# Kernel optimization log

Hardware: AMD Instinct MI355X
Metric: run time of the kernel (lower is better)

Reference implementation:

```python
import jax, jax.numpy as jnp
import numpy as np
import math

N_HEAD = 16
N_HEAD_KV = 4
HEAD_DIM = 128
N_EMBD = 2048

def alibi_slopes(n_heads):
    def pow2_slopes(n):
        start = 2 ** (-2 ** (-(math.log2(n) - 3)))
        return [start * start ** i for i in range(n)]
    if math.log2(n_heads).is_integer():
        return jnp.array(pow2_slopes(n_heads), dtype=jnp.float32)
    closest = 2 ** math.floor(math.log2(n_heads))
    base = pow2_slopes(closest)
    if n_heads <= 2 * closest:
        s = base + base[0::2]
    else:
        s = base + base[0::2] + base[1::2]
    return jnp.array(s[:n_heads], dtype=jnp.float32)

def setup_inputs() -> dict:
    key = jax.random.key(0)
    ks = jax.random.split(key, 5)
    B, T, C = 2, 2048, N_EMBD
    kvdim = N_HEAD_KV * HEAD_DIM
    sc = 0.02
    return {
        "x": jax.random.normal(ks[0], (B, T, C), dtype=jnp.float32),
        "q_w": jax.random.normal(ks[1], (C, C), dtype=jnp.float32) * sc,
        "k_w": jax.random.normal(ks[2], (kvdim, C), dtype=jnp.float32) * sc,
        "v_w": jax.random.normal(ks[3], (kvdim, C), dtype=jnp.float32) * sc,
        "o_w": jax.random.normal(ks[4], (C, C), dtype=jnp.float32) * sc,
    }

def reference(x, q_w, k_w, v_w, o_w):
    B, T, C = x.shape
    H, Hkv, D = N_HEAD, N_HEAD_KV, HEAD_DIM
    # nan/inf sanitize (no-op for random inputs, kept for fidelity)
    x = jnp.nan_to_num(x, nan=0.0, posinf=10000.0, neginf=-10000.0)
    q = (x @ q_w.T).reshape(B, T, H, D).transpose(0, 2, 1, 3)      # [B,H,T,D]
    k = (x @ k_w.T).reshape(B, T, Hkv, D).transpose(0, 2, 1, 3)    # [B,Hkv,T,D]
    v = (x @ v_w.T).reshape(B, T, Hkv, D).transpose(0, 2, 1, 3)
    # repeat_interleave KV heads to H heads
    rep = H // Hkv
    k = jnp.repeat(k, rep, axis=1)
    v = jnp.repeat(v, rep, axis=1)
    scale = 1.0 / math.sqrt(D)
    att = jnp.einsum('bhqd,bhkd->bhqk', q, k) * scale
    att = jnp.clip(att, -10000.0, 10000.0)
    pos = jnp.arange(T)
    causal = jnp.where(pos[None, :] > pos[:, None], -jnp.inf, 0.0)  # [T,T]
    slopes = alibi_slopes(H)  # [H]
    rel = (pos[None, :] - pos[:, None]).astype(jnp.float32)         # [T,T]
    alibi = slopes[:, None, None] * rel[None]                        # [H,T,T]
    att = att + causal[None, None] + alibi[None]
    att = jax.nn.softmax(att.astype(jnp.float32), axis=-1).astype(q.dtype)
    y = jnp.einsum('bhqk,bhkd->bhqd', att, v)
    y = jnp.nan_to_num(y, nan=0.0, posinf=10000.0, neginf=-10000.0)
    y = y.transpose(0, 2, 1, 3).reshape(B, T, C)
    return y @ o_w.T
```

## Files before the change

kernel.cpp:

```cpp
#include <hip/hip_runtime.h>
#include <hip/hip_bf16.h>
#include <math.h>

#define SEQ   2048
#define EMBD  2048
#define NH    16
#define NKV   4
#define HD    128
#define NQKV  3072
#define NUNITS 608
#define NSPLIT 96

typedef __attribute__((ext_vector_type(8))) short short8;
typedef __attribute__((ext_vector_type(4))) short short4v;
typedef __attribute__((ext_vector_type(4))) float floatx4;

static __device__ __forceinline__ short f2bf(float f) {
    union { float f; unsigned u; } cv; cv.f = f;
    unsigned u = cv.u;
    u += 0x7FFF + ((u >> 16) & 1);
    return (short)(u >> 16);
}

#define GL16(gsrc, ldst)                                                        \
    __builtin_amdgcn_global_load_lds(                                           \
        (const __attribute__((address_space(1))) void*)(gsrc),                  \
        (__attribute__((address_space(3))) void*)(ldst), 16, 0, 0)

static __device__ __forceinline__ int alibi_window(float slope2) {
    return (int)ceilf((32.0f / slope2 + 63.0f) * (1.0f / 64.0f));
}

__global__ void cvt_all(const float* __restrict__ x,  const float* __restrict__ qw,
                        const float* __restrict__ kw, const float* __restrict__ vw,
                        const float* __restrict__ ow,
                        short* __restrict__ xb, short* __restrict__ wall,
                        short* __restrict__ owb) {
    int i = blockIdx.x * blockDim.x + threadIdx.x;
    const float* src; short* dst; int off;
    if (i < 2097152)      { src = x;  dst = xb;             off = i; }
    else if (i < 3145728) { src = qw; dst = wall;           off = i - 2097152; }
    else if (i < 3407872) { src = kw; dst = wall + 4194304; off = i - 3145728; }
    else if (i < 3670016) { src = vw; dst = wall + 5242880; off = i - 3407872; }
    else                  { src = ow; dst = owb;            off = i - 3670016; }
    float4 v = ((const float4*)src)[off];
    float a[4] = {v.x, v.y, v.z, v.w};
    short4v o;
#pragma unroll
    for (int j = 0; j < 4; ++j) {
        float f = a[j];
        f = isnan(f) ? 0.0f : fminf(fmaxf(f, -10000.0f), 10000.0f);
        o[j] = f2bf(f);
    }
    ((short4v*)dst)[off] = o;
}

__global__ void attn_setup(int* __restrict__ qtab) {
    __shared__ int keys[NUNITS];
    const int i = threadIdx.x;
    int key = 0, enc = 0;
    if (i < NUNITS) {
        int b, h, p, c;
        if (i < 512) { b = i >> 8; h = (i >> 4) & 15; p = i & 15; c = 0; }
        else { int j = i - 512; b = j / 48; int r2 = j % 48; h = 10 + r2 / 8; p = 8 + r2 % 8; c = 1; }
        float slope2 = exp2f(-0.5f * (float)(h + 1)) * 1.44269504f;
        int W = alibi_window(slope2);
        int L = min(W + 1, 2 * p + 2);
        bool split = (h >= 10) && (p >= 8);
        int n0 = (L + 1) >> 1;
        int cost = split ? (c == 0 ? n0 : L - n0) : L;
        enc = (c << 9) | (b << 8) | (h << 4) | p;
        key = cost * 1024 + i;
        keys[i] = key;
    }
    __syncthreads();
    if (i < NUNITS) {
        int rank = 0;
        for (int j = 0; j < NUNITS; ++j) rank += (keys[j] > key);
        qtab[rank] = enc;
    }
    if (i == 0) qtab[NUNITS] = 0;
}

template<int MODE>
__global__ __launch_bounds__(256) void gemm_bt(
    const short* __restrict__ A, const short* __restrict__ W,
    float* __restrict__ Cout, int M, int N, int K,
    short* __restrict__ qb, short* __restrict__ kb, short* __restrict__ vb)
{
    __shared__ __align__(16) short sA[128 * 64];
    __shared__ __align__(16) short sB[128 * 64];

    const int tid  = threadIdx.x;
    const int lane = tid & 63;
    const int wv   = tid >> 6;
    const int wr   = wv >> 1, wc = wv & 1;
    const int lr   = lane & 15, lg = lane >> 4;
    const int bn   = blockIdx.x, bm = blockIdx.y;

    const short* gA[4]; const short* gB[4];
    short* lA[4]; short* lB[4];
#pragma unroll
    for (int s = 0; s < 4; ++s) {
        int ck  = wv * 256 + s * 64 + lane;
        int row = ck >> 3, seg = ck & 7;
        int segSw = seg ^ (row & 7);
        gA[s] = A + (size_t)(bm * 128 + row) * K + segSw * 8;
        gB[s] = W + (size_t)(bn * 128 + row) * K + segSw * 8;
        lA[s] = &sA[(wv * 256 + s * 64) * 8];
        lB[s] = &sB[(wv * 256 + s * 64) * 8];
    }

    floatx4 acc[4][4] = {};
    const int nkt = K / 64;
    for (int kt = 0; kt < nkt; ++kt) {
#pragma unroll
        for (int s = 0; s < 4; ++s) {
            GL16(gA[s] + kt * 64, lA[s]);
            GL16(gB[s] + kt * 64, lB[s]);
        }
        __syncthreads();

#pragma unroll
        for (int ks = 0; ks < 2; ++ks) {
            short8 af[4], bfr[4];
#pragma unroll
            for (int i = 0; i < 4; ++i) {
                int ra = wr * 64 + i * 16 + lr;
                int rb = wc * 64 + i * 16 + lr;
                af[i]  = *(const short8*)&sA[ra * 64 + (((ks * 4 + lg) ^ (ra & 7)) * 8)];
                bfr[i] = *(const short8*)&sB[rb * 64 + (((ks * 4 + lg) ^ (rb & 7)) * 8)];
            }
#pragma unroll
            for (int i = 0; i < 4; ++i)
#pragma unroll
                for (int j = 0; j < 4; ++j)
                    acc[i][j] = __builtin_amdgcn_mfma_f32_16x16x32_bf16(af[i], bfr[j], acc[i][j], 0, 0, 0);
        }
        __syncthreads();
    }

    const float QSCALE = 0.08838834764831845f * 1.44269504f;
#pragma unroll
    for (int i = 0; i < 4; ++i)
#pragma unroll
        for (int j = 0; j < 4; ++j)
#pragma unroll
            for (int r = 0; r < 4; ++r) {
                int gm = bm * 128 + wr * 64 + i * 16 + lg * 4 + r;
                int gn = bn * 128 + wc * 64 + j * 16 + lr;
                float v = acc[i][j][r];
                if (MODE == 0) {
                    int b = gm >> 11, t = gm & (SEQ - 1);
                    if (gn < 2048) {
                        int h = gn >> 7, d = gn & 127;
                        qb[(((size_t)(b * NH + h)) * SEQ + t) * HD + d] = f2bf(v * QSCALE);
                    } else if (gn < 2560) {
                        int hk = (gn - 2048) >> 7, d = gn & 127;
                        kb[(((size_t)(b * NKV + hk)) * SEQ + t) * HD + d] = f2bf(v);
                    } else {
                        int hv = (gn - 2560) >> 7, d = gn & 127;
                        vb[(((size_t)(b * NKV + hv)) * HD + d) * SEQ + t] = f2bf(v);
                    }
                } else {
                    Cout[(size_t)gm * N + gn] = v;
                }
            }
}

__global__ __launch_bounds__(512, 4) void attn_fwd(
    const short* __restrict__ Q, const short* __restrict__ Kg,
    const short* __restrict__ VT, short* __restrict__ Y,
    float* __restrict__ part, int* __restrict__ qtab)
{
    __shared__ __align__(16) short sK[2][64 * 128];
    __shared__ __align__(16) short sV[128 * 64];
    __shared__ short Plds[8][16][72];
    __shared__ int s_unit;

    const int tid  = threadIdx.x;
    const int wave = tid >> 6, lane = tid & 63;
    const int lr = lane & 15, lg = lane >> 4;
    int* qcnt = qtab + NUNITS;

    int lOff[2];
#pragma unroll
    for (int j = 0; j < 2; ++j)
        lOff[j] = (wave * 128 + j * 64 + lane) * 8;

    for (;;) {
        if (tid == 0) {
            int r = atomicAdd(qcnt, 1);
            s_unit = (r < NUNITS) ? qtab[r] : -1;
        }
        __syncthreads();
        const int enc = s_unit;
        __syncthreads();
        if (enc < 0) break;

        const int c = (enc >> 9) & 1, b = (enc >> 8) & 1;
        const int h = (enc >> 4) & 15, p = enc & 15;
        const int hkv = h >> 2;
        const int qgw = 2 * p + (wave < 4 ? 1 : 0);

        const short* Qb = Q  +  ((size_t)(b * NH  + h  )) * SEQ * HD;
        const short* Kp = Kg +  ((size_t)(b * NKV + hkv)) * SEQ * HD;
        const short* Vp = VT +  ((size_t)(b * NKV + hkv)) * HD * SEQ;

        const float slope2 = exp2f(-0.5f * (float)(h + 1)) * 1.44269504f;
        const int W = alibi_window(slope2);
        const int thi = 2 * p + 1;
        const int L = min(W + 1, 2 * p + 2);
        const bool split = (h >= 10) && (p >= 8);
        const int n0 = (L + 1) >> 1;
        int t1, t0;
        if (!split)      { t1 = thi;      t0 = thi - L + 1; }
        else if (c == 0) { t1 = thi;      t0 = thi - n0 + 1; }
        else             { t1 = thi - n0; t0 = thi - L + 1; }

        const short* gK[2]; const short* gV[2];
#pragma unroll
        for (int j = 0; j < 2; ++j) {
            int ck = wave * 128 + j * 64 + lane;
            int krow = ck >> 4, kseg = ck & 15;
            gK[j] = Kp + (size_t)krow * HD + (kseg ^ (krow & 7)) * 8;
            int vrow = ck >> 3, vseg = ck & 7;
            gV[j] = Vp + (size_t)vrow * SEQ + (vseg ^ (vrow & 7)) * 8;
        }

        float c_nt[4];
#pragma unroll
        for (int nt = 0; nt < 4; ++nt) c_nt[nt] = slope2 * (float)(nt * 16 + lr);

        const int q0 = qgw * 64 + (wave & 3) * 16;
        short8 qf[4];
#pragma unroll
        for (int cc = 0; cc < 4; ++cc)
            qf[cc] = *(const short8*)&Qb[(size_t)(q0 + lr) * HD + cc * 32 + lg * 8];

        floatx4 po[8] = {};
        float m[4], lsum[4];
#pragma unroll
        for (int r = 0; r < 4; ++r) { m[r] = -3.0e38f; lsum[r] = 0.0f; }

        int cur = 0;
#pragma unroll
        for (int j = 0; j < 2; ++j)
            GL16(gK[j] + (size_t)(t1 << 6) * HD, &sK[0][0] + lOff[j]);
        __syncthreads();

#pragma unroll 1
        for (int t = t1; t >= t0; --t) {
#pragma unroll
            for (int j = 0; j < 2; ++j)
                GL16(gV[j] + (t << 6), &sV[0] + lOff[j]);
            if (t > t0) {
#pragma unroll
                for (int j = 0; j < 2; ++j)
                    GL16(gK[j] + (size_t)((t - 1) << 6) * HD, &sK[cur ^ 1][0] + lOff[j]);
            }

            const bool active = (t <= qgw) && (t > qgw - W);
            const int kv0 = t << 6;

            if (active) {
                const short* kr = &sK[cur][0];
                floatx4 sf[4];
                __builtin_amdgcn_s_setprio(1);
#pragma unroll
                for (int nt = 0; nt < 4; ++nt) {
                    floatx4 sacc = {0.f, 0.f, 0.f, 0.f};
#pragma unroll
                    for (int cc = 0; cc < 4; ++cc) {
                        int krow = nt * 16 + lr;
                        short8 kf = *(const short8*)&kr[krow * 128 + (((cc * 4 + lg) ^ (krow & 7)) * 8)];
                        sacc = __builtin_amdgcn_mfma_f32_16x16x32_bf16(qf[cc], kf, sacc, 0, 0, 0);
                    }
                    sf[nt] = sacc;
                }
                __builtin_amdgcn_s_setprio(0);

                const float a2t = slope2 * (float)kv0;
                const bool masked = (t == qgw);
#pragma unroll
                for (int r = 0; r < 4; ++r) {
                    const int qpos = q0 + lg * 4 + r;
                    float sv[4];
#pragma unroll
                    for (int nt = 0; nt < 4; ++nt)
                        sv[nt] = sf[nt][r] + a2t + c_nt[nt];
                    if (masked) {
#pragma unroll
                        for (int nt = 0; nt < 4; ++nt) {
                            int kpos = kv0 + nt * 16 + lr;
                            if (kpos > qpos) sv[nt] = -3.0e38f;
                        }
                    }
                    bool over = (sv[0] > m[r]) | (sv[1] > m[r]) | (sv[2] > m[r]) | (sv[3] > m[r]);
                    if (__any(over)) {
                        float mx = fmaxf(fmaxf(sv[0], sv[1]), fmaxf(sv[2], sv[3]));
#pragma unroll
                        for (int off = 1; off < 16; off <<= 1) mx = fmaxf(mx, __shfl_xor(mx, off));
                        float mn = fmaxf(m[r], mx);
                        float rs = exp2f(m[r] - mn);
                        lsum[r] *= rs;
#pragma unroll
                        for (int dt = 0; dt < 8; ++dt) po[dt][r] *= rs;
                        m[r] = mn;
                    }
#pragma unroll
                    for (int nt = 0; nt < 4; ++nt) {
                        float pp = exp2f(sv[nt] - m[r]);
                        lsum[r] += pp;
                        Plds[wave][lg * 4 + r][nt * 16 + lr] = f2bf(pp);
                    }
                }
            }

            __syncthreads();

            if (active) {
                short8 pf0 = *(const short8*)&Plds[wave][lr][lg * 8];
                short8 pf1 = *(const short8*)&Plds[wave][lr][32 + lg * 8];
                __builtin_amdgcn_s_setprio(1);
#pragma unroll
                for (int dt = 0; dt < 8; ++dt) {
                    int vrow = dt * 16 + lr;
                    short8 vf0 = *(const short8*)&sV[vrow * 64 + (((lg    ) ^ (vrow & 7)) * 8)];
                    short8 vf1 = *(const short8*)&sV[vrow * 64 + (((lg + 4) ^ (vrow & 7)) * 8)];
                    po[dt] = __builtin_amdgcn_mfma_f32_16x16x32_bf16(pf0, vf0, po[dt], 0, 0, 0);
                    po[dt] = __builtin_amdgcn_mfma_f32_16x16x32_bf16(pf1, vf1, po[dt], 0, 0, 0);
                }
                __builtin_amdgcn_s_setprio(0);
            }

            __syncthreads();
            cur ^= 1;
        }

        if (!split) {
#pragma unroll
            for (int r = 0; r < 4; ++r) {
                float sum = lsum[r];
#pragma unroll
                for (int off = 1; off < 16; off <<= 1) sum += __shfl_xor(sum, off);
                float inv = 1.0f / sum;
                int row = q0 + lg * 4 + r;
#pragma unroll
                for (int dt = 0; dt < 8; ++dt)
                    Y[((size_t)(b * SEQ + row)) * EMBD + h * HD + dt * 16 + lr] = f2bf(po[dt][r] * inv);
            }
        } else {
            int jslot = b * 48 + (h - 10) * 8 + (p - 8);
            float* pw = part + (size_t)(jslot * 2 + c) * (128 * 130);
#pragma unroll
            for (int r = 0; r < 4; ++r) {
                float sum = lsum[r];
#pragma unroll
                for (int off = 1; off < 16; off <<= 1) sum += __shfl_xor(sum, off);
                int rr = wave * 16 + lg * 4 + r;
#pragma unroll
                for (int dt = 0; dt < 8; ++dt)
                    pw[rr * 130 + dt * 16 + lr] = po[dt][r];
                if (lr == 0) { pw[rr * 130 + 128] = m[r]; pw[rr * 130 + 129] = sum; }
            }
        }
    }
}

__global__ void attn_combine(const float* __restrict__ part, short* __restrict__ Y) {
    const int tid = threadIdx.x;
    const int rg  = blockIdx.x * 2 + (tid >> 7);
    const int col = tid & 127;
    const int j = rg >> 7, rr = rg & 127;
    const int b = j / 48; const int r2 = j % 48;
    const int h = 10 + r2 / 8, p = 8 + r2 % 8;

    const float* p0 = part + ((size_t)(j * 2) * 128 + rr) * 130;
    const float* p1 = p0 + 128 * 130;
    float m0 = p0[128], l0 = p0[129];
    float m1 = p1[128], l1 = p1[129];
    float M = fmaxf(m0, m1);
    float s0 = exp2f(m0 - M), s1 = exp2f(m1 - M);
    float v = (p0[col] * s0 + p1[col] * s1) / (l0 * s0 + l1 * s1);

    const int w = rr >> 4, i2 = rr & 15;
    const int grow = (w < 4 ? (2 * p + 1) : (2 * p)) * 64 + (w & 3) * 16 + i2;
    Y[((size_t)(b * SEQ + grow)) * EMBD + h * HD + col] = f2bf(v);
}

extern "C" void kernel_launch(void* const* d_in, const int* in_sizes, int n_in,
                              void* d_out, int out_size, void* d_ws, size_t ws_size,
                              hipStream_t stream) {
    const float* x   = (const float*)d_in[0];
    const float* q_w = (const float*)d_in[1];
    const float* k_w = (const float*)d_in[2];
    const float* v_w = (const float*)d_in[3];
    const float* o_w = (const float*)d_in[4];
    float* out = (float*)d_out;

    char* ws = (char*)d_ws;
    short* x_bf  = (short*)(ws);
    short* w_all = (short*)(ws + 16777216);
    short* o_wb  = (short*)(ws + 29360128);
    short* q_b   = (short*)(ws + 37748736);
    short* k_b   = (short*)(ws + 54525952);
    short* vT_b  = (short*)(ws + 58720256);
    short* y_b   = (short*)(ws + 62914560);
    int*   qtab  = (int*)(ws);
    float* part  = (float*)(ws + 65536);

    cvt_all<<<18432, 256, 0, stream>>>(x, q_w, k_w, v_w, o_w, x_bf, w_all, o_wb);

    gemm_bt<0><<<dim3(NQKV / 128, 4096 / 128), 256, 0, stream>>>(
        x_bf, w_all, nullptr, 4096, NQKV, EMBD, q_b, k_b, vT_b);

    attn_setup<<<1, 640, 0, stream>>>(qtab);
    attn_fwd<<<512, 512, 0, stream>>>(q_b, k_b, vT_b, y_b, part, qtab);
    attn_combine<<<6144, 256, 0, stream>>>(part, y_b);

    gemm_bt<1><<<dim3(EMBD / 128, 4096 / 128), 256, 0, stream>>>(
        y_b, o_wb, out, 4096, EMBD, EMBD, nullptr, nullptr, nullptr);
}
```

Before: 201.8 us.

## Double-buffer GEMM LDS tiles with 256x128 blocks and interleaved prefetch

The bf16 GEMM kernel now runs 512 threads on a 256x128 output tile, with the A and B tiles double-buffered in LDS. Global-to-LDS loads for the next k-step are split into chunks and issued between MFMA phases, with s_barrier and setprio around each MFMA burst. This is meant to hide global load latency behind compute and to cut the per-iteration syncthreads stall. In exchange it uses more LDS per block (96KB) and launches fewer blocks for the QKV and output projections, which could lower occupancy and wave count on the CUs.

```diff
diff --git a/kernel.cpp b/kernel.cpp
--- a/kernel.cpp
+++ b/kernel.cpp
@@ -26,6 +26,8 @@
     __builtin_amdgcn_global_load_lds(                                           \
         (const __attribute__((address_space(1))) void*)(gsrc),                  \
         (__attribute__((address_space(3))) void*)(ldst), 16, 0, 0)
+
+#define MFMA16(a, b, c) __builtin_amdgcn_mfma_f32_16x16x32_bf16(a, b, c, 0, 0, 0)
 
 static __device__ __forceinline__ int alibi_window(float slope2) {
     return (int)ceilf((32.0f / slope2 + 63.0f) * (1.0f / 64.0f));
@@ -83,13 +85,13 @@
 }
 
 template<int MODE>
-__global__ __launch_bounds__(256) void gemm_bt(
+__global__ __launch_bounds__(512) void gemm_bt(
     const short* __restrict__ A, const short* __restrict__ W,
     float* __restrict__ Cout, int M, int N, int K,
     short* __restrict__ qb, short* __restrict__ kb, short* __restrict__ vb)
 {
-    __shared__ __align__(16) short sA[128 * 64];
-    __shared__ __align__(16) short sB[128 * 64];
+    __shared__ __align__(16) short sA[2][256 * 64];
+    __shared__ __align__(16) short sB[2][128 * 64];
 
     const int tid  = threadIdx.x;
     const int lane = tid & 63;
@@ -98,46 +100,113 @@
     const int lr   = lane & 15, lg = lane >> 4;
     const int bn   = blockIdx.x, bm = blockIdx.y;
 
-    const short* gA[4]; const short* gB[4];
-    short* lA[4]; short* lB[4];
+    const short* gA[4]; const short* gB[2];
+    int aOff[4], bOff[2];
 #pragma unroll
     for (int s = 0; s < 4; ++s) {
-        int ck  = wv * 256 + s * 64 + lane;
+        int ck = s * 512 + tid;
         int row = ck >> 3, seg = ck & 7;
-        int segSw = seg ^ (row & 7);
-        gA[s] = A + (size_t)(bm * 128 + row) * K + segSw * 8;
-        gB[s] = W + (size_t)(bn * 128 + row) * K + segSw * 8;
-        lA[s] = &sA[(wv * 256 + s * 64) * 8];
-        lB[s] = &sB[(wv * 256 + s * 64) * 8];
+        gA[s] = A + (size_t)(bm * 256 + row) * K + (seg ^ (row & 7)) * 8;
+        aOff[s] = ck * 8;
+    }
+#pragma unroll
+    for (int s = 0; s < 2; ++s) {
+        int ck = s * 512 + tid;
+        int row = ck >> 3, seg = ck & 7;
+        gB[s] = W + (size_t)(bn * 128 + row) * K + (seg ^ (row & 7)) * 8;
+        bOff[s] = ck * 8;
     }
 
     floatx4 acc[4][4] = {};
     const int nkt = K / 64;
+
+#pragma unroll
+    for (int s = 0; s < 4; ++s) GL16(gA[s], &sA[0][0] + aOff[s]);
+#pragma unroll
+    for (int s = 0; s < 2; ++s) GL16(gB[s], &sB[0][0] + bOff[s]);
+    __syncthreads();
+
+#pragma unroll 1
     for (int kt = 0; kt < nkt; ++kt) {
-#pragma unroll
-        for (int s = 0; s < 4; ++s) {
-            GL16(gA[s] + kt * 64, lA[s]);
-            GL16(gB[s] + kt * 64, lB[s]);
+        const int cur = kt & 1;
+        const short* a_ = &sA[cur][0];
+        const short* b_ = &sB[cur][0];
+        short* an = &sA[cur ^ 1][0];
+        short* bnx = &sB[cur ^ 1][0];
+        const bool pf = (kt + 1 < nkt);
+        const int ko = (kt + 1) * 64;
+
+        short8 afA, afB, bfr[4];
+
+        {
+            int ra0 = wr * 64 + lr, ra1 = wr * 64 + 16 + lr;
+            afA = *(const short8*)&a_[ra0 * 64 + ((lg ^ (ra0 & 7)) * 8)];
+            afB = *(const short8*)&a_[ra1 * 64 + ((lg ^ (ra1 & 7)) * 8)];
+#pragma unroll
+            for (int j = 0; j < 4; ++j) {
+                int rb = wc * 64 + j * 16 + lr;
+                bfr[j] = *(const short8*)&b_[rb * 64 + ((lg ^ (rb & 7)) * 8)];
+            }
+            if (pf) { GL16(gA[0] + ko, an + aOff[0]); GL16(gA[1] + ko, an + aOff[1]); }
+            __builtin_amdgcn_s_barrier();
+            __builtin_amdgcn_s_setprio(1);
+#pragma unroll
+            for (int j = 0; j < 4; ++j) {
+                acc[0][j] = MFMA16(afA, bfr[j], acc[0][j]);
+                acc[1][j] = MFMA16(afB, bfr[j], acc[1][j]);
+            }
+            __builtin_amdgcn_s_setprio(0);
+            __builtin_amdgcn_s_barrier();
+        }
+        {
+            int ra2 = wr * 64 + 32 + lr, ra3 = wr * 64 + 48 + lr;
+            afA = *(const short8*)&a_[ra2 * 64 + ((lg ^ (ra2 & 7)) * 8)];
+            afB = *(const short8*)&a_[ra3 * 64 + ((lg ^ (ra3 & 7)) * 8)];
+            if (pf) { GL16(gA[2] + ko, an + aOff[2]); GL16(gA[3] + ko, an + aOff[3]); }
+            __builtin_amdgcn_s_barrier();
+            __builtin_amdgcn_s_setprio(1);
+#pragma unroll
+            for (int j = 0; j < 4; ++j) {
+                acc[2][j] = MFMA16(afA, bfr[j], acc[2][j]);
+                acc[3][j] = MFMA16(afB, bfr[j], acc[3][j]);
+            }
+            __builtin_amdgcn_s_setprio(0);
+            __builtin_amdgcn_s_barrier();
+        }
+        {
+            int ra0 = wr * 64 + lr, ra1 = wr * 64 + 16 + lr;
+            afA = *(const short8*)&a_[ra0 * 64 + (((4 + lg) ^ (ra0 & 7)) * 8)];
+            afB = *(const short8*)&a_[ra1 * 64 + (((4 + lg) ^ (ra1 & 7)) * 8)];
+#pragma unroll
+            for (int j = 0; j < 4; ++j) {
+                int rb = wc * 64 + j * 16 + lr;
+                bfr[j] = *(const short8*)&b_[rb * 64 + (((4 + lg) ^ (rb & 7)) * 8)];
+            }
+            if (pf) { GL16(gB[0] + ko, bnx + bOff[0]); GL16(gB[1] + ko, bnx + bOff[1]); }
+            __builtin_amdgcn_s_barrier();
+            __builtin_amdgcn_s_setprio(1);
+#pragma unroll
+            for (int j = 0; j < 4; ++j) {
+                acc[0][j] = MFMA16(afA, bfr[j], acc[0][j]);
+                acc[1][j] = MFMA16(afB, bfr[j], acc[1][j]);
+            }
+            __builtin_amdgcn_s_setprio(0);
+            __builtin_amdgcn_s_barrier();
+        }
+        {
+            int ra2 = wr * 64 + 32 + lr, ra3 = wr * 64 + 48 + lr;
+            afA = *(const short8*)&a_[ra2 * 64 + (((4 + lg) ^ (ra2 & 7)) * 8)];
+            afB = *(const short8*)&a_[ra3 * 64 + (((4 + lg) ^ (ra3 & 7)) * 8)];
+            __builtin_amdgcn_s_barrier();
+            __builtin_amdgcn_s_setprio(1);
+#pragma unroll
+            for (int j = 0; j < 4; ++j) {
+                acc[2][j] = MFMA16(afA, bfr[j], acc[2][j]);
+                acc[3][j] = MFMA16(afB, bfr[j], acc[3][j]);
+            }
+            __builtin_amdgcn_s_setprio(0);
         }
         __syncthreads();
-
-#pragma unroll
-        for (int ks = 0; ks < 2; ++ks) {
-            short8 af[4], bfr[4];
-#pragma unroll
-            for (int i = 0; i < 4; ++i) {
-                int ra = wr * 64 + i * 16 + lr;
-                int rb = wc * 64 + i * 16 + lr;
-                af[i]  = *(const short8*)&sA[ra * 64 + (((ks * 4 + lg) ^ (ra & 7)) * 8)];
-                bfr[i] = *(const short8*)&sB[rb * 64 + (((ks * 4 + lg) ^ (rb & 7)) * 8)];
-            }
-#pragma unroll
-            for (int i = 0; i < 4; ++i)
-#pragma unroll
-                for (int j = 0; j < 4; ++j)
-                    acc[i][j] = __builtin_amdgcn_mfma_f32_16x16x32_bf16(af[i], bfr[j], acc[i][j], 0, 0, 0);
-        }
-        __syncthreads();
     }
 
     const float QSCALE = 0.08838834764831845f * 1.44269504f;
@@ -147,7 +216,7 @@
         for (int j = 0; j < 4; ++j)
 #pragma unroll
             for (int r = 0; r < 4; ++r) {
-                int gm = bm * 128 + wr * 64 + i * 16 + lg * 4 + r;
+                int gm = bm * 256 + wr * 64 + i * 16 + lg * 4 + r;
                 int gn = bn * 128 + wc * 64 + j * 16 + lr;
                 float v = acc[i][j][r];
                 if (MODE == 0) {
@@ -412,13 +481,13 @@
 
     cvt_all<<<18432, 256, 0, stream>>>(x, q_w, k_w, v_w, o_w, x_bf, w_all, o_wb);
 
-    gemm_bt<0><<<dim3(NQKV / 128, 4096 / 128), 256, 0, stream>>>(
+    gemm_bt<0><<<dim3(NQKV / 128, 4096 / 256), 512, 0, stream>>>(
         x_bf, w_all, nullptr, 4096, NQKV, EMBD, q_b, k_b, vT_b);
 
     attn_setup<<<1, 640, 0, stream>>>(qtab);
     attn_fwd<<<512, 512, 0, stream>>>(q_b, k_b, vT_b, y_b, part, qtab);
     attn_combine<<<6144, 256, 0, stream>>>(part, y_b);
 
-    gemm_bt<1><<<dim3(EMBD / 128, 4096 / 128), 256, 0, stream>>>(
+    gemm_bt<1><<<dim3(EMBD / 128, 4096 / 256), 512, 0, stream>>>(
         y_b, o_wb, out, 4096, EMBD, EMBD, nullptr, nullptr, nullptr);
 }
```

Result: slower. 218.5 us (+8.3%).
